# Optimization experiments

Hardware: AMD Instinct MI355X
Metric: run time of the kernel (lower is better)

The kernel has to match this reference:

```python
import jax, jax.numpy as jnp
import numpy as np

M = 5  # init kwarg of InterestCandidateAttention


def setup_inputs() -> dict:
    key = jax.random.key(0)
    k1, k2, k3 = jax.random.split(key, 3)
    bs, K, d = 4096, 50, 256
    interest = jax.random.normal(k1, (bs, K, d), dtype=jnp.float32)
    candidate = jax.random.normal(k2, (bs, d), dtype=jnp.float32)
    counts = jax.random.randint(k3, (bs,), 1, 20, dtype=jnp.int64)
    return {
        "interest_representations": interest,
        "candidate_news_representation": candidate,
        "unique_category_counts": counts,
    }


def reference(interest_representations, candidate_news_representation, unique_category_counts):
    bs, K, d = interest_representations.shape
    # per-row dot-product scores: [bs, K]
    attn = jnp.einsum("bkd,bd->bk", interest_representations, candidate_news_representation)
    # dynamic K per sample: ceil(log2(M * count)) clamped to [1, K]
    counts = jnp.maximum(unique_category_counts, 1).astype(jnp.float32)
    dyn_K = jnp.clip(jnp.ceil(jnp.log2(M * counts)).astype(jnp.int32), 1, K)  # [bs]
    # rank-based top-k mask (vectorized replacement of per-sample topk loop)
    order = jnp.argsort(-attn, axis=-1)          # indices sorted by descending score
    ranks = jnp.argsort(order, axis=-1)          # rank of each element (0 = largest)
    mask = (ranks < dyn_K[:, None]).astype(attn.dtype)  # [bs, K]
    masked = attn * mask
    # masked weighted sum over interests -> [bs, d]
    user = jnp.einsum("bk,bkd->bd", masked, interest_representations)
    return user
```

## Files before the change

kernel.cpp:

```cpp
#include <hip/hip_runtime.h>

#define NK 50
#define D  256

__global__ __launch_bounds__(256) void ica_kernel(
    const float* __restrict__ interest,
    const float* __restrict__ cand,
    const int*   __restrict__ counts,
    float*       __restrict__ out,
    int bs)
{
    const int b = blockIdx.x;
    if (b >= bs) return;
    const int tid  = threadIdx.x;
    const int lane = tid & 63;
    const int wave = tid >> 6;

    __shared__ float s_attn[NK];
    __shared__ float s_w[NK];
    __shared__ int   s_sel[NK];
    __shared__ int   s_nsel;

    const float* irow_base = interest + (size_t)b * NK * D;

    const float4 c4 = *reinterpret_cast<const float4*>(cand + (size_t)b * D + lane * 4);

    for (int k = wave; k < NK; k += 4) {
        const float4 a4 = *reinterpret_cast<const float4*>(irow_base + (size_t)k * D + lane * 4);
        float p = a4.x * c4.x + a4.y * c4.y + a4.z * c4.z + a4.w * c4.w;
        #pragma unroll
        for (int off = 32; off >= 1; off >>= 1)
            p += __shfl_xor(p, off, 64);
        if (lane == 0) s_attn[k] = p;
    }
    __syncthreads();

    if (wave == 0) {
        int cnt = counts[b];
        if (cnt < 1) cnt = 1;
        int dynK = (int)ceilf(log2f(5.0f * (float)cnt));
        if (dynK < 1)  dynK = 1;
        if (dynK > NK) dynK = NK;

        bool  sel = false;
        if (lane < NK) {
            float my = s_attn[lane];
            int rank = 0;
            #pragma unroll 1
            for (int j = 0; j < NK; ++j) {
                float vj = s_attn[j];
                rank += (vj > my) || (vj == my && j < lane);
            }
            sel = (rank < dynK);
            s_w[lane] = sel ? my : 0.0f;
        }
        unsigned long long m = __ballot(sel);
        if (sel) {
            int pos = __popcll(m & ((1ull << lane) - 1ull));
            s_sel[pos] = lane;
        }
        if (lane == 0) s_nsel = __popcll(m);
    }
    __syncthreads();

    float acc = 0.0f;
    const int n = s_nsel;
    for (int i = 0; i < n; ++i) {
        const int k = s_sel[i];
        acc += s_w[k] * irow_base[(size_t)k * D + tid];
    }
    out[(size_t)b * D + tid] = acc;
}

extern "C" void kernel_launch(void* const* d_in, const int* in_sizes, int n_in,
                              void* d_out, int out_size, void* d_ws, size_t ws_size,
                              hipStream_t stream) {
    const float* interest = (const float*)d_in[0];
    const float* cand     = (const float*)d_in[1];
    const int*   counts   = (const int*)d_in[2];
    float*       out      = (float*)d_out;

    const int bs = in_sizes[2];
    ica_kernel<<<bs, 256, 0, stream>>>(interest, cand, counts, out, bs);
}
```

Baseline: 43.70 us.

## Keep interest rows in registers and reuse them for the weighted sum

Each wave loads its share of interest rows into registers once, uses them for the dot-product scores, then reuses them for the masked weighted sum instead of re-reading the selected rows from memory. The block grows to 8 waves, and per-wave partial sums are combined through shared memory. This removes the second pass over the selected rows, at the cost of more registers and an extra reduction and barrier.

After: 38.28 us. -12.4%, faster.

```diff
diff --git a/kernel.cpp b/kernel.cpp
--- a/kernel.cpp
+++ b/kernel.cpp
@@ -2,36 +2,48 @@
 
 #define NK 50
 #define D  256
+#define NW 8
+#define RPW 7
 
-__global__ __launch_bounds__(256) void ica_kernel(
+__global__ __launch_bounds__(512) void ica_kernel(
     const float* __restrict__ interest,
     const float* __restrict__ cand,
     const int*   __restrict__ counts,
     float*       __restrict__ out,
     int bs)
 {
-    const int b = blockIdx.x;
-    if (b >= bs) return;
+    const int b    = blockIdx.x;
     const int tid  = threadIdx.x;
     const int lane = tid & 63;
     const int wave = tid >> 6;
 
     __shared__ float s_attn[NK];
     __shared__ float s_w[NK];
-    __shared__ int   s_sel[NK];
-    __shared__ int   s_nsel;
+    __shared__ float s_part[NW][D];
 
-    const float* irow_base = interest + (size_t)b * NK * D;
+    const float* irow = interest + (size_t)b * NK * D;
 
     const float4 c4 = *reinterpret_cast<const float4*>(cand + (size_t)b * D + lane * 4);
 
-    for (int k = wave; k < NK; k += 4) {
-        const float4 a4 = *reinterpret_cast<const float4*>(irow_base + (size_t)k * D + lane * 4);
-        float p = a4.x * c4.x + a4.y * c4.y + a4.z * c4.z + a4.w * c4.w;
-        #pragma unroll
-        for (int off = 32; off >= 1; off >>= 1)
-            p += __shfl_xor(p, off, 64);
-        if (lane == 0) s_attn[k] = p;
+    float4 frag[RPW];
+    #pragma unroll
+    for (int i = 0; i < RPW; ++i) {
+        const int k = wave + i * NW;
+        if (k < NK)
+            frag[i] = *reinterpret_cast<const float4*>(irow + (size_t)k * D + lane * 4);
+    }
+
+    #pragma unroll
+    for (int i = 0; i < RPW; ++i) {
+        const int k = wave + i * NW;
+        if (k < NK) {
+            const float4 a4 = frag[i];
+            float p = a4.x * c4.x + a4.y * c4.y + a4.z * c4.z + a4.w * c4.w;
+            #pragma unroll
+            for (int off = 32; off >= 1; off >>= 1)
+                p += __shfl_xor(p, off, 64);
+            if (lane == 0) s_attn[k] = p;
+        }
     }
     __syncthreads();
 
@@ -42,34 +54,41 @@
         if (dynK < 1)  dynK = 1;
         if (dynK > NK) dynK = NK;
 
-        bool  sel = false;
         if (lane < NK) {
-            float my = s_attn[lane];
+            const float my = s_attn[lane];
             int rank = 0;
             #pragma unroll 1
             for (int j = 0; j < NK; ++j) {
-                float vj = s_attn[j];
+                const float vj = s_attn[j];
                 rank += (vj > my) || (vj == my && j < lane);
             }
-            sel = (rank < dynK);
-            s_w[lane] = sel ? my : 0.0f;
+            s_w[lane] = (rank < dynK) ? my : 0.0f;
         }
-        unsigned long long m = __ballot(sel);
-        if (sel) {
-            int pos = __popcll(m & ((1ull << lane) - 1ull));
-            s_sel[pos] = lane;
-        }
-        if (lane == 0) s_nsel = __popcll(m);
     }
     __syncthreads();
 
-    float acc = 0.0f;
-    const int n = s_nsel;
-    for (int i = 0; i < n; ++i) {
-        const int k = s_sel[i];
-        acc += s_w[k] * irow_base[(size_t)k * D + tid];
+    float4 acc = {0.f, 0.f, 0.f, 0.f};
+    #pragma unroll
+    for (int i = 0; i < RPW; ++i) {
+        const int k = wave + i * NW;
+        if (k < NK) {
+            const float w = s_w[k];
+            acc.x += w * frag[i].x;
+            acc.y += w * frag[i].y;
+            acc.z += w * frag[i].z;
+            acc.w += w * frag[i].w;
+        }
     }
-    out[(size_t)b * D + tid] = acc;
+    *reinterpret_cast<float4*>(&s_part[wave][lane * 4]) = acc;
+    __syncthreads();
+
+    if (tid < D) {
+        float r = 0.f;
+        #pragma unroll
+        for (int w = 0; w < NW; ++w)
+            r += s_part[w][tid];
+        out[(size_t)b * D + tid] = r;
+    }
 }
 
 extern "C" void kernel_launch(void* const* d_in, const int* in_sizes, int n_in,
@@ -81,5 +100,5 @@
     float*       out      = (float*)d_out;
 
     const int bs = in_sizes[2];
-    ica_kernel<<<bs, 256, 0, stream>>>(interest, cand, counts, out, bs);
+    ica_kernel<<<bs, 512, 0, stream>>>(interest, cand, counts, out, bs);
 }
```

## Persistent double-buffered kernel keeping interest rows in registers

Applied to the files above, without the earlier changes.

Switches to a persistent grid of 512-thread blocks that loop over samples with register double-buffering, prefetching the next sample's interest rows, candidate and count while computing the current one. The rows stay in registers, so the weighted sum reuses them instead of re-reading selected rows from global memory. Every wave now computes ranks redundantly, and per-wave partial sums are reduced through shared memory. The cost is high register pressure (14 float4 fragments per thread) and extra barriers per sample; it also loads all rows even though only the top-k are needed.

Result: slower. 48.59 us (+11.2%).

```diff
diff --git a/kernel.cpp b/kernel.cpp
--- a/kernel.cpp
+++ b/kernel.cpp
@@ -2,74 +2,107 @@
 
 #define NK 50
 #define D  256
+#define NW 8
+#define RPW 7
+#define GRIDSZ 512
 
-__global__ __launch_bounds__(256) void ica_kernel(
+#define LOAD_SAMPLE(FRAG, C4, CNT, S)                                          \
+    {                                                                          \
+        const float* irow_ = interest + (size_t)(S) * (NK * D);                \
+        _Pragma("unroll")                                                      \
+        for (int i_ = 0; i_ < RPW; ++i_) {                                     \
+            const int k_ = wave + i_ * NW;                                     \
+            if (k_ < NK)                                                       \
+                FRAG[i_] = *reinterpret_cast<const float4*>(                   \
+                    irow_ + (size_t)k_ * D + lane * 4);                        \
+        }                                                                      \
+        C4  = *reinterpret_cast<const float4*>(cand + (size_t)(S) * D + lane * 4); \
+        CNT = counts[S];                                                       \
+    }
+
+#define BODY(FRAG, C4, CNT, P, S, SN, FRAGN, C4N, CNTN)                        \
+    {                                                                          \
+        if ((SN) < bs) LOAD_SAMPLE(FRAGN, C4N, CNTN, SN)                       \
+                                          \
+        _Pragma("unroll")                                                      \
+        for (int i_ = 0; i_ < RPW; ++i_) {                                     \
+            const int k_ = wave + i_ * NW;                                     \
+            if (k_ < NK) {                                                     \
+                const float4 a4 = FRAG[i_];                                    \
+                float p_ = a4.x*C4.x + a4.y*C4.y + a4.z*C4.z + a4.w*C4.w;      \
+                _Pragma("unroll")                                              \
+                for (int off_ = 32; off_ >= 1; off_ >>= 1)                     \
+                    p_ += __shfl_xor(p_, off_, 64);                            \
+                if (lane == 0) s_attn[P][k_] = p_;                             \
+            }                                                                  \
+        }                                                                      \
+        __syncthreads();                                                       \
+        int cnt_ = CNT; if (cnt_ < 1) cnt_ = 1;                                \
+        int dynK_ = (int)ceilf(log2f(5.0f * (float)cnt_));                     \
+        if (dynK_ < 1)  dynK_ = 1;                                             \
+        if (dynK_ > NK) dynK_ = NK;                                            \
+        const float my_ = (lane < NK) ? s_attn[P][lane] : 0.0f;                \
+        int rank_ = 0;                                                         \
+        _Pragma("unroll")                                                      \
+        for (int j_ = 0; j_ < NK; ++j_) {                                      \
+            const float vj_ = s_attn[P][j_];                                   \
+            rank_ += (vj_ > my_) || (vj_ == my_ && j_ < lane);                 \
+        }                                                                      \
+        const float wsel_ = (lane < NK && rank_ < dynK_) ? my_ : 0.0f;         \
+        float4 acc_ = {0.f, 0.f, 0.f, 0.f};                                    \
+        _Pragma("unroll")                                                      \
+        for (int i_ = 0; i_ < RPW; ++i_) {                                     \
+            const int k_ = wave + i_ * NW;                                     \
+            if (k_ < NK) {                                                     \
+                const float w_ = __shfl(wsel_, k_, 64);                        \
+                acc_.x += w_ * FRAG[i_].x;  acc_.y += w_ * FRAG[i_].y;         \
+                acc_.z += w_ * FRAG[i_].z;  acc_.w += w_ * FRAG[i_].w;         \
+            }                                                                  \
+        }                                                                      \
+        *reinterpret_cast<float4*>(&s_part[P][wave][lane * 4]) = acc_;         \
+        __syncthreads();                                                       \
+        if (tid < D) {                                                         \
+            float r_ = 0.f;                                                    \
+            _Pragma("unroll")                                                  \
+            for (int w_ = 0; w_ < NW; ++w_) r_ += s_part[P][w_][tid];          \
+            out[(size_t)(S) * D + tid] = r_;                                   \
+        }                                                                      \
+    }
+
+__global__ __launch_bounds__(512, 4) void ica_kernel(
     const float* __restrict__ interest,
     const float* __restrict__ cand,
     const int*   __restrict__ counts,
     float*       __restrict__ out,
     int bs)
 {
-    const int b = blockIdx.x;
-    if (b >= bs) return;
     const int tid  = threadIdx.x;
     const int lane = tid & 63;
     const int wave = tid >> 6;
+    const int stride = gridDim.x;
 
-    __shared__ float s_attn[NK];
-    __shared__ float s_w[NK];
-    __shared__ int   s_sel[NK];
-    __shared__ int   s_nsel;
+    __shared__ float s_attn[2][NK];
+    __shared__ float s_part[2][NW][D];
 
-    const float* irow_base = interest + (size_t)b * NK * D;
+    float4 fragA[RPW], fragB[RPW];
+    float4 c4A, c4B;
+    int    cntA, cntB;
 
-    const float4 c4 = *reinterpret_cast<const float4*>(cand + (size_t)b * D + lane * 4);
+    int s = blockIdx.x;
+    if (s >= bs) return;
 
-    for (int k = wave; k < NK; k += 4) {
-        const float4 a4 = *reinterpret_cast<const float4*>(irow_base + (size_t)k * D + lane * 4);
-        float p = a4.x * c4.x + a4.y * c4.y + a4.z * c4.z + a4.w * c4.w;
-        #pragma unroll
-        for (int off = 32; off >= 1; off >>= 1)
-            p += __shfl_xor(p, off, 64);
-        if (lane == 0) s_attn[k] = p;
+    LOAD_SAMPLE(fragA, c4A, cntA, s)
+
+    #pragma unroll 1
+    for (;;) {
+        const int sB = s + stride;
+        BODY(fragA, c4A, cntA, 0, s, sB, fragB, c4B, cntB)
+        if (sB >= bs) break;
+        const int sA = sB + stride;
+        BODY(fragB, c4B, cntB, 1, sB, sA, fragA, c4A, cntA)
+        if (sA >= bs) break;
+        s = sA;
     }
-    __syncthreads();
-
-    if (wave == 0) {
-        int cnt = counts[b];
-        if (cnt < 1) cnt = 1;
-        int dynK = (int)ceilf(log2f(5.0f * (float)cnt));
-        if (dynK < 1)  dynK = 1;
-        if (dynK > NK) dynK = NK;
-
-        bool  sel = false;
-        if (lane < NK) {
-            float my = s_attn[lane];
-            int rank = 0;
-            #pragma unroll 1
-            for (int j = 0; j < NK; ++j) {
-                float vj = s_attn[j];
-                rank += (vj > my) || (vj == my && j < lane);
-            }
-            sel = (rank < dynK);
-            s_w[lane] = sel ? my : 0.0f;
-        }
-        unsigned long long m = __ballot(sel);
-        if (sel) {
-            int pos = __popcll(m & ((1ull << lane) - 1ull));
-            s_sel[pos] = lane;
-        }
-        if (lane == 0) s_nsel = __popcll(m);
-    }
-    __syncthreads();
-
-    float acc = 0.0f;
-    const int n = s_nsel;
-    for (int i = 0; i < n; ++i) {
-        const int k = s_sel[i];
-        acc += s_w[k] * irow_base[(size_t)k * D + tid];
-    }
-    out[(size_t)b * D + tid] = acc;
 }
 
 extern "C" void kernel_launch(void* const* d_in, const int* in_sizes, int n_in,
@@ -80,6 +113,7 @@
     const int*   counts   = (const int*)d_in[2];
     float*       out      = (float*)d_out;
 
-    const int bs = in_sizes[2];
-    ica_kernel<<<bs, 256, 0, stream>>>(interest, cand, counts, out, bs);
+    const int bs   = in_sizes[2];
+    const int grid = (bs < GRIDSZ) ? bs : GRIDSZ;
+    ica_kernel<<<grid, 512, 0, stream>>>(interest, cand, counts, out, bs);
 }
```
